# Kernel optimization log

Hardware: AMD Instinct MI355X
Metric: run time of the kernel (lower is better)

## Reference

```python
import jax, jax.numpy as jnp
import numpy as np

MAX_BITS = 64
HIDDEN = 256
EPS = 1e-5
TEMPERATURE = 1.0  # buffer default


def _layernorm(x, gamma, beta):
    mu = jnp.mean(x, axis=-1, keepdims=True)
    var = jnp.var(x, axis=-1, keepdims=True)
    return (x - mu) * jax.lax.rsqrt(var + EPS) * gamma + beta


def setup_inputs() -> dict:
    key = jax.random.key(0)
    ks = jax.random.split(key, 8)
    B = 32768
    # binary-ish inputs in [0,1)
    a_bits = (jax.random.uniform(ks[0], (B, MAX_BITS)) < 0.5).astype(jnp.float32)
    shift_bits = (jax.random.uniform(ks[1], (B, MAX_BITS)) < 0.5).astype(jnp.float32)
    # decoder: Linear(64,256) -> LN -> ReLU -> Linear(256,256) -> LN -> ReLU -> Linear(256,64)
    def lin(k, out_d, in_d):
        bound = 1.0 / np.sqrt(in_d)
        kw, kb = jax.random.split(k)
        W = jax.random.uniform(kw, (out_d, in_d), minval=-bound, maxval=bound)
        b = jax.random.uniform(kb, (out_d,), minval=-bound, maxval=bound)
        return W, b
    W1, b1 = lin(ks[2], HIDDEN, MAX_BITS)
    W2, b2 = lin(ks[3], HIDDEN, HIDDEN)
    W3, b3 = lin(ks[4], MAX_BITS, HIDDEN)
    g1 = jnp.ones((HIDDEN,)); be1 = jnp.zeros((HIDDEN,))
    g2 = jnp.ones((HIDDEN,)); be2 = jnp.zeros((HIDDEN,))
    return {
        "a_bits": a_bits, "shift_bits": shift_bits,
        "W1": W1, "b1": b1, "g1": g1, "be1": be1,
        "W2": W2, "b2": b2, "g2": g2, "be2": be2,
        "W3": W3, "b3": b3,
    }


def reference(a_bits, shift_bits, W1, b1, g1, be1, W2, b2, g2, be2, W3, b3):
    bits = a_bits.shape[1]
    # 2-layer MLP decoder
    h = jax.nn.relu(_layernorm(shift_bits @ W1.T + b1, g1, be1))
    h = jax.nn.relu(_layernorm(h @ W2.T + b2, g2, be2))
    shift_logits = (h @ W3.T + b3)[:, :bits]
    # training path: softmax over shift positions
    shift_probs = jax.nn.softmax(shift_logits / TEMPERATURE, axis=-1)
    # Toeplitz shift-sum: out[b,i] = sum_{s<=i} probs[b,s] * a_bits[b,i-s]
    i = jnp.arange(bits)[:, None]
    s = jnp.arange(bits)[None, :]
    idx = i - s                       # [bits, bits]
    mask = (idx >= 0)
    gath = a_bits[:, jnp.where(mask, idx, 0)] * mask.astype(a_bits.dtype)  # [B, bits, bits]
    return jnp.einsum('bis,bs->bi', gath, shift_probs)
```

## Files before the change

kernel.cpp:

```cpp
#include <hip/hip_runtime.h>
#include <hip/hip_fp16.h>


typedef short s8v __attribute__((ext_vector_type(8)));
typedef float f4v __attribute__((ext_vector_type(4)));

#define HPAD 264
#define PPAD 68

#define OFF_W1F 0
#define OFF_W2F 16384
#define OFF_W3F 81920
#define OFF_B1  98304
#define OFF_G1  98560
#define OFF_BE1 98816
#define OFF_B2  99072
#define OFF_G2  99328
#define OFF_BE2 99584
#define OFF_B3  99840

__device__ __forceinline__ float b2f(unsigned short u) {
    union { unsigned int i; float f; } v; v.i = ((unsigned int)u) << 16; return v.f;
}
__device__ __forceinline__ unsigned short f2b(float f) {
    union { float f; unsigned int i; } v; v.f = f;
    return (unsigned short)((v.i + 0x7fffu + ((v.i >> 16) & 1u)) >> 16);
}
__device__ __forceinline__ int h2i(__half2 h) { union { __half2 h; int i; } u; u.h = h; return u.i; }
__device__ __forceinline__ __half2 i2h(int i) { union { __half2 h; int i; } u; u.i = i; return u.h; }

__device__ __forceinline__ bool probe_bf16(const void* a_bits) {
    unsigned int wv = ((const unsigned int*)a_bits)[threadIdx.x & 63];
    return __ballot((wv & 0xffffu) == 0x3f80u) != 0ULL;
}

__global__ __launch_bounds__(256) void convert_kernel(
    const void* __restrict__ a_probe,
    const void* __restrict__ W1, const void* __restrict__ W2, const void* __restrict__ W3,
    const void* __restrict__ b1, const void* __restrict__ g1, const void* __restrict__ be1,
    const void* __restrict__ b2, const void* __restrict__ g2, const void* __restrict__ be2,
    const void* __restrict__ b3,
    unsigned short* __restrict__ ws)
{
    const bool isbf = probe_bf16(a_probe);
    const int t = blockIdx.x * 256 + threadIdx.x;

    if (t < 12288) {
        const void* W; int K, idx, dstbase;
        if (t < 2048)       { idx = t;         W = W1; K = 64;  dstbase = OFF_W1F + idx * 8; }
        else if (t < 10240) { idx = t - 2048;  W = W2; K = 256; dstbase = OFF_W2F + idx * 8; }
        else                { idx = t - 10240; W = W3; K = 256; dstbase = OFF_W3F + idx * 8; }
        int nt, kc, lane;
        if (t < 2048) { nt = idx >> 7; kc = (idx >> 6) & 1; lane = idx & 63; }
        else          { nt = idx >> 9; kc = (idx >> 6) & 7; lane = idx & 63; }
        const int row = nt * 16 + (lane & 15);
        const int col = kc * 32 + (lane >> 4) * 8;
        const int src = row * K + col;
        s8v o;
        if (isbf) {
            o = *(const s8v*)((const unsigned short*)W + src);
        } else {
            const float* f = (const float*)W + src;
#pragma unroll
            for (int j = 0; j < 8; ++j) o[j] = (short)f2b(f[j]);
        }
        *(s8v*)(ws + dstbase) = o;
    } else if (t < 12488) {
        const int v = t - 12288;
        const void* srcp; int base, off;
        if (v < 32)       { srcp = b1;  base = OFF_B1;  off = v * 8; }
        else if (v < 64)  { srcp = g1;  base = OFF_G1;  off = (v - 32) * 8; }
        else if (v < 96)  { srcp = be1; base = OFF_BE1; off = (v - 64) * 8; }
        else if (v < 128) { srcp = b2;  base = OFF_B2;  off = (v - 96) * 8; }
        else if (v < 160) { srcp = g2;  base = OFF_G2;  off = (v - 128) * 8; }
        else if (v < 192) { srcp = be2; base = OFF_BE2; off = (v - 160) * 8; }
        else              { srcp = b3;  base = OFF_B3;  off = (v - 192) * 8; }
#pragma unroll
        for (int j = 0; j < 8; ++j)
            ws[base + off + j] = isbf ? ((const unsigned short*)srcp)[off + j]
                                      : f2b(((const float*)srcp)[off + j]);
    }
}

template<bool BF16>
__device__ __forceinline__ float loadS(const void* p, int idx) {
    if constexpr (BF16) return b2f(((const unsigned short*)p)[idx]);
    else return ((const float*)p)[idx];
}
template<bool BF16>
__device__ __forceinline__ s8v loadA8(const void* p, int idx) {
    if constexpr (BF16) {
        return *(const s8v*)((const unsigned short*)p + idx);
    } else {
        const float* f = (const float*)p + idx;
        f4v a = *(const f4v*)f;
        f4v b = *(const f4v*)(f + 4);
        s8v r;
#pragma unroll
        for (int i = 0; i < 4; ++i) { r[i] = (short)f2b(a[i]); r[4 + i] = (short)f2b(b[i]); }
        return r;
    }
}
template<bool BF16>
__device__ __forceinline__ void storeO(void* p, int idx, float v) {
    if constexpr (BF16) ((unsigned short*)p)[idx] = f2b(v);
    else ((float*)p)[idx] = v;
}

template<bool BF16>
__device__ __forceinline__ void pipeline(
    const void* a_bits, const void* shifts, const unsigned short* ws, void* out,
    short* Hs, float* Ps, float* SS)
{
    const int tid = threadIdx.x;
    const int w = tid >> 6;
    const int band = w >> 1;
    const int h = w & 1;
    const int l = tid & 63;
    const int q = l >> 4;
    const int c = l & 15;
    const int rb = band << 4;
    const int ntb = h << 3;
    const int grow0 = (int)blockIdx.x << 5;
    float* myS = SS + ((band * 2 + h) * 16) * 2;
    float* otS = SS + ((band * 2 + (1 - h)) * 16) * 2;

    f4v acc1[8];
#pragma unroll
    for (int i = 0; i < 8; ++i) acc1[i] = (f4v){0.f, 0.f, 0.f, 0.f};

    const s8v xa0 = loadA8<BF16>(shifts, (grow0 + rb + c) * 64 + q * 8);
    const s8v xa1 = loadA8<BF16>(shifts, (grow0 + rb + c) * 64 + 32 + q * 8);
#pragma unroll
    for (int i = 0; i < 8; ++i) {
        const int nt = ntb + i;
        s8v wb0 = *(const s8v*)(ws + OFF_W1F + ((nt * 2 + 0) * 64 + l) * 8);
        s8v wb1 = *(const s8v*)(ws + OFF_W1F + ((nt * 2 + 1) * 64 + l) * 8);
        acc1[i] = __builtin_amdgcn_mfma_f32_16x16x32_bf16(xa0, wb0, acc1[i], 0, 0, 0);
        acc1[i] = __builtin_amdgcn_mfma_f32_16x16x32_bf16(xa1, wb1, acc1[i], 0, 0, 0);
    }
    {
        float s[4] = {0, 0, 0, 0}, ss[4] = {0, 0, 0, 0};
#pragma unroll
        for (int i = 0; i < 8; ++i) {
            float bias = b2f(ws[OFF_B1 + (ntb + i) * 16 + c]);
#pragma unroll
            for (int r = 0; r < 4; ++r) {
                float v = acc1[i][r] + bias;
                acc1[i][r] = v;
                s[r] += v; ss[r] += v * v;
            }
        }
#pragma unroll
        for (int m = 1; m <= 8; m <<= 1)
#pragma unroll
            for (int r = 0; r < 4; ++r) {
                s[r]  += __shfl_xor(s[r],  m, 64);
                ss[r] += __shfl_xor(ss[r], m, 64);
            }
        if (c == 0)
#pragma unroll
            for (int r = 0; r < 4; ++r) {
                myS[(q * 4 + r) * 2 + 0] = s[r];
                myS[(q * 4 + r) * 2 + 1] = ss[r];
            }
        __syncthreads();
#pragma unroll
        for (int r = 0; r < 4; ++r) {
            float st = s[r] + otS[(q * 4 + r) * 2 + 0];
            float sq = ss[r] + otS[(q * 4 + r) * 2 + 1];
            float mean = st * (1.0f / 256.0f);
            float var  = fmaxf(sq * (1.0f / 256.0f) - mean * mean, 0.0f);
            s[r] = mean; ss[r] = rsqrtf(var + 1e-5f);
        }
#pragma unroll
        for (int i = 0; i < 8; ++i) {
            const int nt = ntb + i;
            float gg = b2f(ws[OFF_G1 + nt * 16 + c]);
            float bb = b2f(ws[OFF_BE1 + nt * 16 + c]);
#pragma unroll
            for (int r = 0; r < 4; ++r) {
                float y = (acc1[i][r] - s[r]) * ss[r] * gg + bb;
                Hs[(rb + q * 4 + r) * HPAD + nt * 16 + c] = (short)f2b(fmaxf(y, 0.0f));
            }
        }
    }
    __syncthreads();

    f4v acc2[8];
#pragma unroll
    for (int i = 0; i < 8; ++i) acc2[i] = (f4v){0.f, 0.f, 0.f, 0.f};
#pragma unroll
    for (int ks = 0; ks < 8; ++ks) {
        s8v af = *(const s8v*)&Hs[(rb + c) * HPAD + ks * 32 + q * 8];
#pragma unroll
        for (int i = 0; i < 8; ++i) {
            const int nt = ntb + i;
            s8v bf_ = *(const s8v*)(ws + OFF_W2F + ((nt * 8 + ks) * 64 + l) * 8);
            acc2[i] = __builtin_amdgcn_mfma_f32_16x16x32_bf16(af, bf_, acc2[i], 0, 0, 0);
        }
    }
    {
        float s[4] = {0, 0, 0, 0}, ss[4] = {0, 0, 0, 0};
#pragma unroll
        for (int i = 0; i < 8; ++i) {
            float bias = b2f(ws[OFF_B2 + (ntb + i) * 16 + c]);
#pragma unroll
            for (int r = 0; r < 4; ++r) {
                float v = acc2[i][r] + bias;
                acc2[i][r] = v;
                s[r] += v; ss[r] += v * v;
            }
        }
#pragma unroll
        for (int m = 1; m <= 8; m <<= 1)
#pragma unroll
            for (int r = 0; r < 4; ++r) {
                s[r]  += __shfl_xor(s[r],  m, 64);
                ss[r] += __shfl_xor(ss[r], m, 64);
            }
        if (c == 0)
#pragma unroll
            for (int r = 0; r < 4; ++r) {
                myS[(q * 4 + r) * 2 + 0] = s[r];
                myS[(q * 4 + r) * 2 + 1] = ss[r];
            }
        __syncthreads();
#pragma unroll
        for (int r = 0; r < 4; ++r) {
            float st = s[r] + otS[(q * 4 + r) * 2 + 0];
            float sq = ss[r] + otS[(q * 4 + r) * 2 + 1];
            float mean = st * (1.0f / 256.0f);
            float var  = fmaxf(sq * (1.0f / 256.0f) - mean * mean, 0.0f);
            s[r] = mean; ss[r] = rsqrtf(var + 1e-5f);
        }
#pragma unroll
        for (int i = 0; i < 8; ++i) {
            const int nt = ntb + i;
            float gg = b2f(ws[OFF_G2 + nt * 16 + c]);
            float bb = b2f(ws[OFF_BE2 + nt * 16 + c]);
#pragma unroll
            for (int r = 0; r < 4; ++r) {
                float y = (acc2[i][r] - s[r]) * ss[r] * gg + bb;
                Hs[(rb + q * 4 + r) * HPAD + nt * 16 + c] = (short)f2b(fmaxf(y, 0.0f));
            }
        }
    }
    __syncthreads();

    f4v acc3[4];
#pragma unroll
    for (int nt = 0; nt < 4; ++nt) acc3[nt] = (f4v){0.f, 0.f, 0.f, 0.f};
#pragma unroll
    for (int ks = 0; ks < 8; ++ks) {
        s8v af = *(const s8v*)&Hs[(rb + c) * HPAD + ks * 32 + q * 8];
#pragma unroll
        for (int nt = 0; nt < 4; ++nt) {
            s8v bf_ = *(const s8v*)(ws + OFF_W3F + ((nt * 8 + ks) * 64 + l) * 8);
            acc3[nt] = __builtin_amdgcn_mfma_f32_16x16x32_bf16(af, bf_, acc3[nt], 0, 0, 0);
        }
    }
    __syncthreads();
    {
        float mx[4] = {-1e30f, -1e30f, -1e30f, -1e30f};
#pragma unroll
        for (int nt = 0; nt < 4; ++nt) {
            float bias = b2f(ws[OFF_B3 + nt * 16 + c]);
#pragma unroll
            for (int r = 0; r < 4; ++r) {
                float v = acc3[nt][r] + bias;
                acc3[nt][r] = v;
                mx[r] = fmaxf(mx[r], v);
            }
        }
#pragma unroll
        for (int m = 1; m <= 8; m <<= 1)
#pragma unroll
            for (int r = 0; r < 4; ++r)
                mx[r] = fmaxf(mx[r], __shfl_xor(mx[r], m, 64));
        float sum[4] = {0, 0, 0, 0};
#pragma unroll
        for (int nt = 0; nt < 4; ++nt)
#pragma unroll
            for (int r = 0; r < 4; ++r) {
                float e = __expf(acc3[nt][r] - mx[r]);
                acc3[nt][r] = e;
                sum[r] += e;
            }
#pragma unroll
        for (int m = 1; m <= 8; m <<= 1)
#pragma unroll
            for (int r = 0; r < 4; ++r)
                sum[r] += __shfl_xor(sum[r], m, 64);
#pragma unroll
        for (int r = 0; r < 4; ++r) sum[r] = 1.0f / sum[r];
        if (h == 0)
#pragma unroll
            for (int nt = 0; nt < 4; ++nt)
#pragma unroll
                for (int r = 0; r < 4; ++r)
                    Ps[(rb + q * 4 + r) * PPAD + nt * 16 + c] = acc3[nt][r] * sum[r];
    }
    __syncthreads();

#pragma unroll 2
    for (int jj = 0; jj < 4; ++jj) {
        const int j = h * 4 + jj;
        const int m0 = rb + j, m1 = rb + j + 8;
        __half2 pph = __floats2half2_rn(Ps[m0 * PPAD + l], Ps[m1 * PPAD + l]);
        const int ppi = h2i(pph);
        __half2 aah = __floats2half2_rn(loadS<BF16>(a_bits, (grow0 + m0) * 64 + l),
                                        loadS<BF16>(a_bits, (grow0 + m1) * 64 + l));
        int r = h2i(aah);
        __half2 acc = __float2half2_rn(0.0f);
#pragma unroll
        for (int s = 0; s < 64; ++s) {
            const int spi = __builtin_amdgcn_readlane(ppi, s);
            acc = __hfma2(i2h(spi), i2h(r), acc);
            if (s < 63)
                r = __builtin_amdgcn_update_dpp(0, r, 0x138, 0xF, 0xF, true);
        }
        storeO<BF16>(out, (grow0 + m0) * 64 + l, __low2float(acc));
        storeO<BF16>(out, (grow0 + m1) * 64 + l, __high2float(acc));
    }
}

__global__ __launch_bounds__(256, 4) void shiftdec_kernel(
    const void* __restrict__ a_bits, const void* __restrict__ shifts,
    const unsigned short* __restrict__ ws, void* __restrict__ out)
{
    __shared__ __align__(16) char smem[32 * HPAD * 2];
    __shared__ __align__(16) float SSb[2 * 2 * 16 * 2];
    short* Hs = (short*)smem;
    float* Ps = (float*)smem;

    if (probe_bf16(a_bits))
        pipeline<true>(a_bits, shifts, ws, out, Hs, Ps, SSb);
    else
        pipeline<false>(a_bits, shifts, ws, out, Hs, Ps, SSb);
}

extern "C" void kernel_launch(void* const* d_in, const int* in_sizes, int n_in,
                              void* d_out, int out_size, void* d_ws, size_t ws_size,
                              hipStream_t stream) {
    const int B = in_sizes[0] / 64;
    const int grid = B / 32;

    hipLaunchKernelGGL(convert_kernel, dim3(49), dim3(256), 0, stream,
                       d_in[0], d_in[2], d_in[6], d_in[10],
                       d_in[3], d_in[4], d_in[5], d_in[7], d_in[8], d_in[9], d_in[11],
                       (unsigned short*)d_ws);
    hipLaunchKernelGGL(shiftdec_kernel, dim3(grid), dim3(256), 0, stream,
                       d_in[0], d_in[1], (const unsigned short*)d_ws, d_out);
}
```

Measured before the change: 117.5 us.

## Split 16-row tile across four waves by output columns, doubling block count

Each block now handles 16 rows instead of 32. The four waves split the hidden and output columns four ways rather than two bands times two halves, and the grid doubles. LayerNorm statistics and the softmax max and sum are now reduced across all four waves through shared memory. That adds extra __syncthreads but halves per-wave accumulator registers and allows a higher occupancy target (launch bounds 8). The cost is that each wave re-streams the full weight matrices for fewer rows, which lowers weight reuse per block.

```diff
diff --git a/kernel.cpp b/kernel.cpp
--- a/kernel.cpp
+++ b/kernel.cpp
@@ -113,26 +113,22 @@
     short* Hs, float* Ps, float* SS)
 {
     const int tid = threadIdx.x;
-    const int w = tid >> 6;
-    const int band = w >> 1;
-    const int h = w & 1;
+    const int h = tid >> 6;
     const int l = tid & 63;
     const int q = l >> 4;
     const int c = l & 15;
-    const int rb = band << 4;
-    const int ntb = h << 3;
-    const int grow0 = (int)blockIdx.x << 5;
-    float* myS = SS + ((band * 2 + h) * 16) * 2;
-    float* otS = SS + ((band * 2 + (1 - h)) * 16) * 2;
-
-    f4v acc1[8];
-#pragma unroll
-    for (int i = 0; i < 8; ++i) acc1[i] = (f4v){0.f, 0.f, 0.f, 0.f};
-
-    const s8v xa0 = loadA8<BF16>(shifts, (grow0 + rb + c) * 64 + q * 8);
-    const s8v xa1 = loadA8<BF16>(shifts, (grow0 + rb + c) * 64 + 32 + q * 8);
-#pragma unroll
-    for (int i = 0; i < 8; ++i) {
+    const int ntb = h << 2;
+    const int grow0 = (int)blockIdx.x << 4;
+    const int row = q * 4;
+
+    f4v acc1[4];
+#pragma unroll
+    for (int i = 0; i < 4; ++i) acc1[i] = (f4v){0.f, 0.f, 0.f, 0.f};
+
+    const s8v xa0 = loadA8<BF16>(shifts, (grow0 + c) * 64 + q * 8);
+    const s8v xa1 = loadA8<BF16>(shifts, (grow0 + c) * 64 + 32 + q * 8);
+#pragma unroll
+    for (int i = 0; i < 4; ++i) {
         const int nt = ntb + i;
         s8v wb0 = *(const s8v*)(ws + OFF_W1F + ((nt * 2 + 0) * 64 + l) * 8);
         s8v wb1 = *(const s8v*)(ws + OFF_W1F + ((nt * 2 + 1) * 64 + l) * 8);
@@ -142,7 +138,7 @@
     {
         float s[4] = {0, 0, 0, 0}, ss[4] = {0, 0, 0, 0};
 #pragma unroll
-        for (int i = 0; i < 8; ++i) {
+        for (int i = 0; i < 4; ++i) {
             float bias = b2f(ws[OFF_B1 + (ntb + i) * 16 + c]);
 #pragma unroll
             for (int r = 0; r < 4; ++r) {
@@ -161,40 +157,44 @@
         if (c == 0)
 #pragma unroll
             for (int r = 0; r < 4; ++r) {
-                myS[(q * 4 + r) * 2 + 0] = s[r];
-                myS[(q * 4 + r) * 2 + 1] = ss[r];
+                SS[(h * 16 + row + r) * 2 + 0] = s[r];
+                SS[(h * 16 + row + r) * 2 + 1] = ss[r];
             }
         __syncthreads();
 #pragma unroll
         for (int r = 0; r < 4; ++r) {
-            float st = s[r] + otS[(q * 4 + r) * 2 + 0];
-            float sq = ss[r] + otS[(q * 4 + r) * 2 + 1];
+            float st = 0.f, sq = 0.f;
+#pragma unroll
+            for (int wv = 0; wv < 4; ++wv) {
+                st += SS[(wv * 16 + row + r) * 2 + 0];
+                sq += SS[(wv * 16 + row + r) * 2 + 1];
+            }
             float mean = st * (1.0f / 256.0f);
             float var  = fmaxf(sq * (1.0f / 256.0f) - mean * mean, 0.0f);
             s[r] = mean; ss[r] = rsqrtf(var + 1e-5f);
         }
 #pragma unroll
-        for (int i = 0; i < 8; ++i) {
+        for (int i = 0; i < 4; ++i) {
             const int nt = ntb + i;
             float gg = b2f(ws[OFF_G1 + nt * 16 + c]);
             float bb = b2f(ws[OFF_BE1 + nt * 16 + c]);
 #pragma unroll
             for (int r = 0; r < 4; ++r) {
                 float y = (acc1[i][r] - s[r]) * ss[r] * gg + bb;
-                Hs[(rb + q * 4 + r) * HPAD + nt * 16 + c] = (short)f2b(fmaxf(y, 0.0f));
+                Hs[(row + r) * HPAD + nt * 16 + c] = (short)f2b(fmaxf(y, 0.0f));
             }
         }
     }
     __syncthreads();
 
-    f4v acc2[8];
-#pragma unroll
-    for (int i = 0; i < 8; ++i) acc2[i] = (f4v){0.f, 0.f, 0.f, 0.f};
+    f4v acc2[4];
+#pragma unroll
+    for (int i = 0; i < 4; ++i) acc2[i] = (f4v){0.f, 0.f, 0.f, 0.f};
 #pragma unroll
     for (int ks = 0; ks < 8; ++ks) {
-        s8v af = *(const s8v*)&Hs[(rb + c) * HPAD + ks * 32 + q * 8];
-#pragma unroll
-        for (int i = 0; i < 8; ++i) {
+        s8v af = *(const s8v*)&Hs[c * HPAD + ks * 32 + q * 8];
+#pragma unroll
+        for (int i = 0; i < 4; ++i) {
             const int nt = ntb + i;
             s8v bf_ = *(const s8v*)(ws + OFF_W2F + ((nt * 8 + ks) * 64 + l) * 8);
             acc2[i] = __builtin_amdgcn_mfma_f32_16x16x32_bf16(af, bf_, acc2[i], 0, 0, 0);
@@ -203,7 +203,7 @@
     {
         float s[4] = {0, 0, 0, 0}, ss[4] = {0, 0, 0, 0};
 #pragma unroll
-        for (int i = 0; i < 8; ++i) {
+        for (int i = 0; i < 4; ++i) {
             float bias = b2f(ws[OFF_B2 + (ntb + i) * 16 + c]);
 #pragma unroll
             for (int r = 0; r < 4; ++r) {
@@ -222,115 +222,122 @@
         if (c == 0)
 #pragma unroll
             for (int r = 0; r < 4; ++r) {
-                myS[(q * 4 + r) * 2 + 0] = s[r];
-                myS[(q * 4 + r) * 2 + 1] = ss[r];
+                SS[(h * 16 + row + r) * 2 + 0] = s[r];
+                SS[(h * 16 + row + r) * 2 + 1] = ss[r];
             }
         __syncthreads();
 #pragma unroll
         for (int r = 0; r < 4; ++r) {
-            float st = s[r] + otS[(q * 4 + r) * 2 + 0];
-            float sq = ss[r] + otS[(q * 4 + r) * 2 + 1];
+            float st = 0.f, sq = 0.f;
+#pragma unroll
+            for (int wv = 0; wv < 4; ++wv) {
+                st += SS[(wv * 16 + row + r) * 2 + 0];
+                sq += SS[(wv * 16 + row + r) * 2 + 1];
+            }
             float mean = st * (1.0f / 256.0f);
             float var  = fmaxf(sq * (1.0f / 256.0f) - mean * mean, 0.0f);
             s[r] = mean; ss[r] = rsqrtf(var + 1e-5f);
         }
 #pragma unroll
-        for (int i = 0; i < 8; ++i) {
+        for (int i = 0; i < 4; ++i) {
             const int nt = ntb + i;
             float gg = b2f(ws[OFF_G2 + nt * 16 + c]);
             float bb = b2f(ws[OFF_BE2 + nt * 16 + c]);
 #pragma unroll
             for (int r = 0; r < 4; ++r) {
                 float y = (acc2[i][r] - s[r]) * ss[r] * gg + bb;
-                Hs[(rb + q * 4 + r) * HPAD + nt * 16 + c] = (short)f2b(fmaxf(y, 0.0f));
+                Hs[(row + r) * HPAD + nt * 16 + c] = (short)f2b(fmaxf(y, 0.0f));
             }
         }
     }
     __syncthreads();
 
-    f4v acc3[4];
-#pragma unroll
-    for (int nt = 0; nt < 4; ++nt) acc3[nt] = (f4v){0.f, 0.f, 0.f, 0.f};
+    f4v acc3 = (f4v){0.f, 0.f, 0.f, 0.f};
 #pragma unroll
     for (int ks = 0; ks < 8; ++ks) {
-        s8v af = *(const s8v*)&Hs[(rb + c) * HPAD + ks * 32 + q * 8];
-#pragma unroll
-        for (int nt = 0; nt < 4; ++nt) {
-            s8v bf_ = *(const s8v*)(ws + OFF_W3F + ((nt * 8 + ks) * 64 + l) * 8);
-            acc3[nt] = __builtin_amdgcn_mfma_f32_16x16x32_bf16(af, bf_, acc3[nt], 0, 0, 0);
-        }
-    }
-    __syncthreads();
+        s8v af = *(const s8v*)&Hs[c * HPAD + ks * 32 + q * 8];
+        s8v bf_ = *(const s8v*)(ws + OFF_W3F + ((h * 8 + ks) * 64 + l) * 8);
+        acc3 = __builtin_amdgcn_mfma_f32_16x16x32_bf16(af, bf_, acc3, 0, 0, 0);
+    }
     {
-        float mx[4] = {-1e30f, -1e30f, -1e30f, -1e30f};
-#pragma unroll
-        for (int nt = 0; nt < 4; ++nt) {
-            float bias = b2f(ws[OFF_B3 + nt * 16 + c]);
-#pragma unroll
-            for (int r = 0; r < 4; ++r) {
-                float v = acc3[nt][r] + bias;
-                acc3[nt][r] = v;
-                mx[r] = fmaxf(mx[r], v);
-            }
-        }
+        float mx = -1e30f;
+        const float bias = b2f(ws[OFF_B3 + h * 16 + c]);
+#pragma unroll
+        for (int r = 0; r < 4; ++r) {
+            acc3[r] += bias;
+            mx = fmaxf(mx, acc3[r]);
+        }
+        float mxr[4];
+#pragma unroll
+        for (int r = 0; r < 4; ++r) mxr[r] = acc3[r];
 #pragma unroll
         for (int m = 1; m <= 8; m <<= 1)
 #pragma unroll
             for (int r = 0; r < 4; ++r)
-                mx[r] = fmaxf(mx[r], __shfl_xor(mx[r], m, 64));
-        float sum[4] = {0, 0, 0, 0};
-#pragma unroll
-        for (int nt = 0; nt < 4; ++nt)
-#pragma unroll
-            for (int r = 0; r < 4; ++r) {
-                float e = __expf(acc3[nt][r] - mx[r]);
-                acc3[nt][r] = e;
-                sum[r] += e;
-            }
+                mxr[r] = fmaxf(mxr[r], __shfl_xor(mxr[r], m, 64));
+        if (c == 0)
+#pragma unroll
+            for (int r = 0; r < 4; ++r)
+                SS[(h * 16 + row + r) * 2 + 0] = mxr[r];
+        __syncthreads();
+        float sum[4];
+#pragma unroll
+        for (int r = 0; r < 4; ++r) {
+            float M = SS[(0 * 16 + row + r) * 2 + 0];
+            M = fmaxf(M, SS[(1 * 16 + row + r) * 2 + 0]);
+            M = fmaxf(M, SS[(2 * 16 + row + r) * 2 + 0]);
+            M = fmaxf(M, SS[(3 * 16 + row + r) * 2 + 0]);
+            float e = __expf(acc3[r] - M);
+            acc3[r] = e;
+            sum[r] = e;
+        }
 #pragma unroll
         for (int m = 1; m <= 8; m <<= 1)
 #pragma unroll
             for (int r = 0; r < 4; ++r)
                 sum[r] += __shfl_xor(sum[r], m, 64);
-#pragma unroll
-        for (int r = 0; r < 4; ++r) sum[r] = 1.0f / sum[r];
-        if (h == 0)
-#pragma unroll
-            for (int nt = 0; nt < 4; ++nt)
-#pragma unroll
-                for (int r = 0; r < 4; ++r)
-                    Ps[(rb + q * 4 + r) * PPAD + nt * 16 + c] = acc3[nt][r] * sum[r];
+        if (c == 0)
+#pragma unroll
+            for (int r = 0; r < 4; ++r)
+                SS[(h * 16 + row + r) * 2 + 1] = sum[r];
+        __syncthreads();
+#pragma unroll
+        for (int r = 0; r < 4; ++r) {
+            float S = SS[(0 * 16 + row + r) * 2 + 1] + SS[(1 * 16 + row + r) * 2 + 1]
+                    + SS[(2 * 16 + row + r) * 2 + 1] + SS[(3 * 16 + row + r) * 2 + 1];
+            Ps[(row + r) * PPAD + h * 16 + c] = acc3[r] / S;
+        }
     }
     __syncthreads();
 
-#pragma unroll 2
-    for (int jj = 0; jj < 4; ++jj) {
-        const int j = h * 4 + jj;
-        const int m0 = rb + j, m1 = rb + j + 8;
+#pragma unroll
+    for (int jj = 0; jj < 2; ++jj) {
+        const int j = h * 2 + jj;
+        const int m0 = j, m1 = j + 8;
         __half2 pph = __floats2half2_rn(Ps[m0 * PPAD + l], Ps[m1 * PPAD + l]);
         const int ppi = h2i(pph);
         __half2 aah = __floats2half2_rn(loadS<BF16>(a_bits, (grow0 + m0) * 64 + l),
                                         loadS<BF16>(a_bits, (grow0 + m1) * 64 + l));
-        int r = h2i(aah);
+        int rr = h2i(aah);
         __half2 acc = __float2half2_rn(0.0f);
 #pragma unroll
         for (int s = 0; s < 64; ++s) {
             const int spi = __builtin_amdgcn_readlane(ppi, s);
-            acc = __hfma2(i2h(spi), i2h(r), acc);
+            acc = __hfma2(i2h(spi), i2h(rr), acc);
             if (s < 63)
-                r = __builtin_amdgcn_update_dpp(0, r, 0x138, 0xF, 0xF, true);
+                rr = __builtin_amdgcn_update_dpp(0, rr, 0x138, 0xF, 0xF, true);
         }
         storeO<BF16>(out, (grow0 + m0) * 64 + l, __low2float(acc));
         storeO<BF16>(out, (grow0 + m1) * 64 + l, __high2float(acc));
     }
 }
 
-__global__ __launch_bounds__(256, 4) void shiftdec_kernel(
+__global__ __launch_bounds__(256, 8) void shiftdec_kernel(
     const void* __restrict__ a_bits, const void* __restrict__ shifts,
     const unsigned short* __restrict__ ws, void* __restrict__ out)
 {
-    __shared__ __align__(16) char smem[32 * HPAD * 2];
-    __shared__ __align__(16) float SSb[2 * 2 * 16 * 2];
+    __shared__ __align__(16) char smem[16 * HPAD * 2];
+    __shared__ __align__(16) float SSb[4 * 16 * 2];
     short* Hs = (short*)smem;
     float* Ps = (float*)smem;
 
@@ -344,7 +351,7 @@
                               void* d_out, int out_size, void* d_ws, size_t ws_size,
                               hipStream_t stream) {
     const int B = in_sizes[0] / 64;
-    const int grid = B / 32;
+    const int grid = B / 16;
 
     hipLaunchKernelGGL(convert_kernel, dim3(49), dim3(256), 0, stream,
                        d_in[0], d_in[2], d_in[6], d_in[10],
```

After: 116.6 us. About the same (-0.7%).
